# Performance work log

Hardware: AMD Instinct MI355X
Metric: run time of the kernel (lower is better)

The kernel has to match this reference:

```python
import jax, jax.numpy as jnp
import numpy as np

NUM_GROUPS = 32
EPS = 1e-6


def group_norm(x, w, b):
    # x: (B, C, L); normalize per group of C//32 channels over (channels-in-group, L)
    B, C, L = x.shape
    xg = x.reshape(B, NUM_GROUPS, C // NUM_GROUPS, L)
    mean = jnp.mean(xg, axis=(2, 3), keepdims=True)
    var = jnp.var(xg, axis=(2, 3), keepdims=True)
    xn = ((xg - mean) * jax.lax.rsqrt(var + EPS)).reshape(B, C, L)
    return xn * w[None, :, None] + b[None, :, None]


def conv1x1(x, w, b):
    # 1x1 Conv1d == channel-mixing linear. x: (B,C,L), w: (O,C), b: (O,)
    return jnp.einsum('oc,bcl->bol', w, x) + b[None, :, None]


def setup_inputs() -> dict:
    key = jax.random.key(0)
    ks = jax.random.split(key, 6)
    B, C, L = 8, 512, 2048
    s = 1.0 / np.sqrt(C)
    return {
        'x': jax.random.normal(ks[0], (B, C, L), dtype=jnp.float32),
        'gn_w': jnp.ones((C,), jnp.float32),
        'gn_b': jnp.zeros((C,), jnp.float32),
        'wq': jax.random.normal(ks[1], (C, C), dtype=jnp.float32) * s,
        'bq': jnp.zeros((C,), jnp.float32),
        'wk': jax.random.normal(ks[2], (C, C), dtype=jnp.float32) * s,
        'bk': jnp.zeros((C,), jnp.float32),
        'wv': jax.random.normal(ks[3], (C, C), dtype=jnp.float32) * s,
        'bv': jnp.zeros((C,), jnp.float32),
        'wo': jax.random.normal(ks[4], (C, C), dtype=jnp.float32) * s,
        'bo': jnp.zeros((C,), jnp.float32),
    }


def reference(x, gn_w, gn_b, wq, bq, wk, bk, wv, bv, wo, bo):
    B, C, L = x.shape
    h = group_norm(x, gn_w, gn_b)
    q = conv1x1(h, wq, bq)  # (B,C,L)
    k = conv1x1(h, wk, bk)
    v = conv1x1(h, wv, bv)
    scale = jnp.asarray(C, x.dtype) ** -0.5
    # scores over length: w[b,i,j] = sum_c q[b,c,i] k[b,c,j]
    w_ = jnp.einsum('bci,bcj->bij', q, k) * scale
    w_ = jax.nn.softmax(w_, axis=-1)
    # h[b,c,i] = sum_j w[b,i,j] v[b,c,j]
    h = jnp.einsum('bij,bcj->bci', w_, v)
    h = conv1x1(h, wo, bo)
    return x + h
```

## Files before the change

### kernel.cpp

```cpp
#include <hip/hip_runtime.h>
#include <math.h>

#define BATCH 8
#define CH 512
#define LEN 2048
#define NG 32
#define CPG 16

typedef unsigned short u16;
typedef __bf16 bf16x8 __attribute__((ext_vector_type(8)));
typedef float f32x16 __attribute__((ext_vector_type(16)));

__device__ __forceinline__ u16 f2bf(float f) {
    union { float f; unsigned u; } c; c.f = f;
    unsigned r = c.u + 0x7fffu + ((c.u >> 16) & 1u);
    return (u16)(r >> 16);
}
__device__ __forceinline__ float bf2f(u16 h) {
    union { unsigned u; float f; } c; c.u = ((unsigned)h) << 16;
    return c.f;
}
__device__ __forceinline__ void gload16(const u16* g, u16* l) {
    __builtin_amdgcn_global_load_lds(
        (const __attribute__((address_space(1))) unsigned int*)g,
        (__attribute__((address_space(3))) unsigned int*)l, 16, 0, 0);
}

__global__ __launch_bounds__(256) void zerof4(float4* __restrict__ p) {
    p[blockIdx.x * 256 + threadIdx.x] = make_float4(0.f, 0.f, 0.f, 0.f);
}

__global__ __launch_bounds__(256) void wconv4(const float* __restrict__ w0, const float* __restrict__ w1,
                                              const float* __restrict__ w2, const float* __restrict__ w3,
                                              u16* __restrict__ o0, u16* __restrict__ o1,
                                              u16* __restrict__ o2, u16* __restrict__ o3) {
    const float* s; u16* d;
    switch (blockIdx.y) {
        case 0: s = w0; d = o0; break;
        case 1: s = w1; d = o1; break;
        case 2: s = w2; d = o2; break;
        default: s = w3; d = o3; break;
    }
    const int i = blockIdx.x * 256 + threadIdx.x;
    float4 f = ((const float4*)s)[i];
    ushort4 o = make_ushort4(f2bf(f.x), f2bf(f.y), f2bf(f.z), f2bf(f.w));
    ((ushort4*)d)[i] = o;
}

__global__ __launch_bounds__(256) void gn_stats_p(const float* __restrict__ x,
                                                  float* __restrict__ stats) {
    const int blk = blockIdx.x;
    const int b = blk >> 7, g = (blk >> 2) & 31, sl = blk & 3;
    const float4* xp = (const float4*)(x + ((size_t)b * CH + (size_t)g * CPG) * LEN) + sl * 2048;
    float s = 0.f, s2 = 0.f;
    #pragma unroll
    for (int i = 0; i < 8; ++i) {
        float4 v = xp[threadIdx.x + i * 256];
        s += v.x + v.y + v.z + v.w;
        s2 = fmaf(v.x, v.x, fmaf(v.y, v.y, fmaf(v.z, v.z, fmaf(v.w, v.w, s2))));
    }
    #pragma unroll
    for (int off = 32; off > 0; off >>= 1) {
        s  += __shfl_down(s, off, 64);
        s2 += __shfl_down(s2, off, 64);
    }
    __shared__ float sm[2][4];
    const int lane = threadIdx.x & 63, wv = threadIdx.x >> 6;
    if (lane == 0) { sm[0][wv] = s; sm[1][wv] = s2; }
    __syncthreads();
    if (threadIdx.x == 0) {
        atomicAdd(&stats[b * NG + g],       sm[0][0] + sm[0][1] + sm[0][2] + sm[0][3]);
        atomicAdd(&stats[256 + b * NG + g], sm[1][0] + sm[1][1] + sm[1][2] + sm[1][3]);
    }
}

__global__ __launch_bounds__(256) void gn_fin(const float* __restrict__ stats,
                                              const float* __restrict__ gw,
                                              const float* __restrict__ gb,
                                              float* __restrict__ gnA,
                                              float* __restrict__ gnB) {
    const int idx = blockIdx.x * 256 + threadIdx.x;
    const int b = idx >> 9, c = idx & 511, g = c >> 4;
    const float S  = stats[b * NG + g];
    const float S2 = stats[256 + b * NG + g];
    const float mean = S * (1.f / (CPG * LEN));
    const float var  = S2 * (1.f / (CPG * LEN)) - mean * mean;
    const float a = rsqrtf(var + 1e-6f) * gw[c];
    gnA[idx] = a;
    gnB[idx] = gb[c] - mean * a;
}

__global__ __launch_bounds__(256) void gn_apply_t(const float* __restrict__ x,
                                                  const float* __restrict__ gnA,
                                                  const float* __restrict__ gnB,
                                                  u16* __restrict__ Ht) {
    __shared__ float tile[64][65];
    const int b = blockIdx.z, c0 = blockIdx.y * 64, l0 = blockIdx.x * 64;
    const int t = threadIdx.x, tl = t & 63, tr = t >> 6;
    #pragma unroll 4
    for (int i = 0; i < 16; ++i) {
        const int c = tr + i * 4;
        const float a = gnA[b * CH + c0 + c];
        const float sh = gnB[b * CH + c0 + c];
        tile[c][tl] = x[((size_t)b * CH + c0 + c) * LEN + l0 + tl] * a + sh;
    }
    __syncthreads();
    #pragma unroll 4
    for (int i = 0; i < 16; ++i) {
        const int l = tr + i * 4;
        Ht[((size_t)b * LEN + l0 + l) * CH + c0 + tl] = f2bf(tile[tl][l]);
    }
}

#define EPI_QK   0
#define EPI_TBN  1
#define EPI_EXP  2
#define EPI_TNRM 3
#define EPI_FIN  4

template <int MODE>
__global__ __launch_bounds__(256, 4) void gemm_bt(
    const u16* __restrict__ A, int lda, long long sA,
    const u16* __restrict__ B, int ldb, long long sB,
    void* __restrict__ Out, void* __restrict__ Out2,
    int ldo, long long sO,
    const float* __restrict__ bias, const float* __restrict__ bias2,
    const float* __restrict__ res, long long sR,
    float* __restrict__ rsum, long long sRS,
    int K, float alpha) {
    __shared__ u16 As[128 * 64];
    __shared__ u16 Bs[128 * 64];

    int bz, by, bx;
    if (MODE == EPI_EXP) {
        const int gx = gridDim.x, gy = gridDim.y;
        int flat = (blockIdx.z * gy + blockIdx.y) * gx + blockIdx.x;
        const int nbk = gx * gy * (int)gridDim.z;
        flat = (flat & 7) * (nbk >> 3) + (flat >> 3);
        bz = flat / (gx * gy);
        const int rr = flat - bz * gx * gy;
        by = rr / gx;
        bx = rr - by * gx;
    } else {
        bz = blockIdx.z; by = blockIdx.y; bx = blockIdx.x;
    }

    const int n0 = bx * 128, m0 = by * 128;
    A += (size_t)bz * sA;
    B += (size_t)bz * sB;
    const int t = threadIdx.x;
    const int lane = t & 63, wid = t >> 6;

    const int rowL = t >> 3, kq = (t & 7) ^ (rowL & 7);
    unsigned aoff = (unsigned)((m0 + rowL) * lda + kq * 8);
    unsigned boff = (unsigned)((n0 + rowL) * ldb + kq * 8);
    u16* const lds_dst_a = As + t * 8;
    u16* const lds_dst_b = Bs + t * 8;

    f32x16 acc[2][2];
    #pragma unroll
    for (int i = 0; i < 2; ++i)
        #pragma unroll
        for (int j = 0; j < 2; ++j)
            acc[i][j] = (f32x16)(0.f);

    const int col = lane & 31, half = lane >> 5;
    const int wm = (wid & 1) * 64, wn = (wid >> 1) * 64;
    const int mf = wm + col, nf = wn + col;
    const int mswz = mf & 7, nswz = nf & 7;

    for (int k0 = 0; k0 < K; k0 += 64) {
        #pragma unroll
        for (int g = 0; g < 4; ++g) {
            gload16(A + aoff + g * (32 * lda), lds_dst_a + g * 2048);
            gload16(B + boff + g * (32 * ldb), lds_dst_b + g * 2048);
        }
        aoff += 64; boff += 64;
        __syncthreads();
        #pragma unroll
        for (int ks = 0; ks < 4; ++ks) {
            const int kcA = ((ks * 2 + half) ^ mswz) * 8;
            const int kcB = ((ks * 2 + half) ^ nswz) * 8;
            bf16x8 a0 = *(const bf16x8*)(As + (mf)      * 64 + kcA);
            bf16x8 a1 = *(const bf16x8*)(As + (mf + 32) * 64 + kcA);
            bf16x8 b0 = *(const bf16x8*)(Bs + (nf)      * 64 + kcB);
            bf16x8 b1 = *(const bf16x8*)(Bs + (nf + 32) * 64 + kcB);
            acc[0][0] = __builtin_amdgcn_mfma_f32_32x32x16_bf16(a0, b0, acc[0][0], 0, 0, 0);
            acc[0][1] = __builtin_amdgcn_mfma_f32_32x32x16_bf16(a0, b1, acc[0][1], 0, 0, 0);
            acc[1][0] = __builtin_amdgcn_mfma_f32_32x32x16_bf16(a1, b0, acc[1][0], 0, 0, 0);
            acc[1][1] = __builtin_amdgcn_mfma_f32_32x32x16_bf16(a1, b1, acc[1][1], 0, 0, 0);
        }
        __syncthreads();
    }

    if (MODE == EPI_FIN) {
        float* O = (float*)Out + (size_t)bz * sO;
        const float* R = res + (size_t)bz * sR;
        #pragma unroll
        for (int im = 0; im < 2; ++im)
            #pragma unroll
            for (int g4 = 0; g4 < 4; ++g4) {
                const int mb = m0 + wm + im * 32 + g4 * 8 + half * 4;
                #pragma unroll
                for (int jn = 0; jn < 2; ++jn) {
                    const int n = n0 + wn + jn * 32 + col;
                    const float bb = bias[n];
                    const size_t base = (size_t)n * ldo + mb;
                    const float4 r4 = *(const float4*)&R[base];
                    float4 o4;
                    o4.x = acc[im][jn][g4 * 4 + 0] + bb + r4.x;
                    o4.y = acc[im][jn][g4 * 4 + 1] + bb + r4.y;
                    o4.z = acc[im][jn][g4 * 4 + 2] + bb + r4.z;
                    o4.w = acc[im][jn][g4 * 4 + 3] + bb + r4.w;
                    *(float4*)&O[base] = o4;
                }
            }
    } else if (MODE == EPI_EXP) {
        u16* O = (u16*)Out + (size_t)bz * sO;
        float* RS = rsum + (size_t)bz * sRS;
        float psum[2] = {0.f, 0.f};
        #pragma unroll
        for (int im = 0; im < 2; ++im)
            #pragma unroll
            for (int g4 = 0; g4 < 4; ++g4) {
                const int mb = m0 + wm + im * 32 + g4 * 8 + half * 4;
                #pragma unroll
                for (int jn = 0; jn < 2; ++jn) {
                    const int n = n0 + wn + jn * 32 + col;
                    u16 h0 = f2bf(__expf(acc[im][jn][g4 * 4 + 0] * alpha));
                    u16 h1 = f2bf(__expf(acc[im][jn][g4 * 4 + 1] * alpha));
                    u16 h2 = f2bf(__expf(acc[im][jn][g4 * 4 + 2] * alpha));
                    u16 h3 = f2bf(__expf(acc[im][jn][g4 * 4 + 3] * alpha));
                    psum[jn] += bf2f(h0) + bf2f(h1) + bf2f(h2) + bf2f(h3);
                    *(ushort4*)&O[(size_t)n * ldo + mb] = make_ushort4(h0, h1, h2, h3);
                }
            }
        #pragma unroll
        for (int jn = 0; jn < 2; ++jn) psum[jn] += __shfl_xor(psum[jn], 32, 64);
        if (half == 0) {
            #pragma unroll
            for (int jn = 0; jn < 2; ++jn)
                atomicAdd(&RS[n0 + wn + jn * 32 + col], psum[jn]);
        }
    } else {
        u16* O;
        const float* bi = bias;
        const float* RS = (MODE == EPI_TNRM) ? rsum + (size_t)bz * sRS : nullptr;
        int mbase = m0 + wm;
        if (MODE == EPI_QK) {
            const bool hi = (m0 & 512) != 0;
            O  = (u16*)(hi ? Out2 : Out) + (size_t)bz * sO;
            bi = hi ? bias2 : bias;
            mbase = (m0 & 511) + wm;
        } else {
            O = (u16*)Out + (size_t)bz * sO;
        }
        float inv[2];
        if (MODE == EPI_TNRM) {
            inv[0] = 1.f / RS[n0 + wn + col];
            inv[1] = 1.f / RS[n0 + wn + 32 + col];
        }
        #pragma unroll
        for (int im = 0; im < 2; ++im)
            #pragma unroll
            for (int g4 = 0; g4 < 4; ++g4) {
                const int mb = mbase + im * 32 + g4 * 8 + half * 4;
                float4 bm = make_float4(0.f, 0.f, 0.f, 0.f);
                if (MODE == EPI_QK) bm = *(const float4*)&bi[mb];
                #pragma unroll
                for (int jn = 0; jn < 2; ++jn) {
                    const int n = n0 + wn + jn * 32 + col;
                    float v0 = acc[im][jn][g4 * 4 + 0];
                    float v1 = acc[im][jn][g4 * 4 + 1];
                    float v2 = acc[im][jn][g4 * 4 + 2];
                    float v3 = acc[im][jn][g4 * 4 + 3];
                    if (MODE == EPI_QK)  { v0 += bm.x; v1 += bm.y; v2 += bm.z; v3 += bm.w; }
                    if (MODE == EPI_TBN) { const float bb = bi[n]; v0 += bb; v1 += bb; v2 += bb; v3 += bb; }
                    if (MODE == EPI_TNRM) { v0 *= inv[jn]; v1 *= inv[jn]; v2 *= inv[jn]; v3 *= inv[jn]; }
                    ushort4 pk = make_ushort4(f2bf(v0), f2bf(v1), f2bf(v2), f2bf(v3));
                    *(ushort4*)&O[(size_t)n * ldo + mb] = pk;
                }
            }
    }
}

extern "C" void kernel_launch(void* const* d_in, const int* in_sizes, int n_in,
                              void* d_out, int out_size, void* d_ws, size_t ws_size,
                              hipStream_t stream) {
    const float* x    = (const float*)d_in[0];
    const float* gn_w = (const float*)d_in[1];
    const float* gn_b = (const float*)d_in[2];
    const float* wq   = (const float*)d_in[3];
    const float* bq   = (const float*)d_in[4];
    const float* wk   = (const float*)d_in[5];
    const float* bk   = (const float*)d_in[6];
    const float* wv   = (const float*)d_in[7];
    const float* bv   = (const float*)d_in[8];
    const float* wo   = (const float*)d_in[9];
    const float* bo   = (const float*)d_in[10];
    float* out = (float*)d_out;

    char* p = (char*)d_ws;
    const size_t WSZ = (size_t)CH * CH * 2;
    const size_t HSZ = (size_t)BATCH * CH * LEN * 2;
    u16* Wqk = (u16*)p; p += 2 * WSZ;
    u16* Wvb = (u16*)p; p += WSZ;
    u16* Wob = (u16*)p; p += WSZ;
    u16* Ht  = (u16*)p; p += HSZ;
    u16* Qt  = (u16*)p; p += HSZ;
    u16* Kt  = (u16*)p; p += HSZ;
    u16* Vb  = (u16*)p; p += HSZ;
    u16* Sb  = (u16*)p; p += (size_t)BATCH * LEN * LEN * 2;
    float* gnA = (float*)p; p += (size_t)BATCH * CH * 4;
    float* gnB = (float*)p; p += (size_t)BATCH * CH * 4;
    float* rowsum = (float*)p; p += (size_t)BATCH * LEN * 4;
    float* stats  = (float*)p;

    const long long sH = (long long)LEN * CH;
    const long long sV = (long long)CH * LEN;
    const long long sS = (long long)LEN * LEN;
    const float scale = 0.04419417382415922f;

    zerof4<<<17, 256, 0, stream>>>((float4*)rowsum);
    wconv4<<<dim3(256, 4), 256, 0, stream>>>(wq, wk, wv, wo,
                                             Wqk, Wqk + (size_t)CH * CH, Wvb, Wob);
    gn_stats_p<<<BATCH * NG * 4, 256, 0, stream>>>(x, stats);
    gn_fin<<<BATCH * CH / 256, 256, 0, stream>>>(stats, gn_w, gn_b, gnA, gnB);
    gn_apply_t<<<dim3(LEN / 64, CH / 64, BATCH), 256, 0, stream>>>(x, gnA, gnB, Ht);

    gemm_bt<EPI_QK><<<dim3(16, 8, 8), 256, 0, stream>>>(
        Wqk, CH, 0, Ht, CH, sH, Qt, Kt, CH, sH, bq, bk, nullptr, 0, nullptr, 0, CH, 0.f);
    gemm_bt<EPI_TBN><<<dim3(4, 16, 8), 256, 0, stream>>>(
        Ht, CH, sH, Wvb, CH, 0, Vb, nullptr, LEN, sV, bv, nullptr, nullptr, 0, nullptr, 0, CH, 0.f);
    gemm_bt<EPI_EXP><<<dim3(16, 16, 8), 256, 0, stream>>>(
        Kt, CH, sH, Qt, CH, sH, Sb, nullptr, LEN, sS, nullptr, nullptr, nullptr, 0, rowsum, LEN, CH, scale);
    gemm_bt<EPI_TNRM><<<dim3(16, 4, 8), 256, 0, stream>>>(
        Vb, LEN, sV, Sb, LEN, sS, Ht, nullptr, CH, sH, nullptr, nullptr, nullptr, 0, rowsum, LEN, LEN, 0.f);
    gemm_bt<EPI_FIN><<<dim3(4, 16, 8), 256, 0, stream>>>(
        Ht, CH, sH, Wob, CH, 0, out, nullptr, LEN, sV, bo, nullptr, x, sV, nullptr, 0, CH, 0.f);
}
```

Baseline: 275.8 us.

## Fuse preprocessing kernels and fold group-norm finalize into the transpose-apply kernel

```diff
diff --git a/kernel.cpp b/kernel.cpp
--- a/kernel.cpp
+++ b/kernel.cpp
@@ -26,89 +26,94 @@
         (__attribute__((address_space(3))) unsigned int*)l, 16, 0, 0);
 }
 
-__global__ __launch_bounds__(256) void zerof4(float4* __restrict__ p) {
-    p[blockIdx.x * 256 + threadIdx.x] = make_float4(0.f, 0.f, 0.f, 0.f);
-}
-
-__global__ __launch_bounds__(256) void wconv4(const float* __restrict__ w0, const float* __restrict__ w1,
-                                              const float* __restrict__ w2, const float* __restrict__ w3,
-                                              u16* __restrict__ o0, u16* __restrict__ o1,
-                                              u16* __restrict__ o2, u16* __restrict__ o3) {
-    const float* s; u16* d;
-    switch (blockIdx.y) {
-        case 0: s = w0; d = o0; break;
-        case 1: s = w1; d = o1; break;
-        case 2: s = w2; d = o2; break;
-        default: s = w3; d = o3; break;
-    }
-    const int i = blockIdx.x * 256 + threadIdx.x;
-    float4 f = ((const float4*)s)[i];
-    ushort4 o = make_ushort4(f2bf(f.x), f2bf(f.y), f2bf(f.z), f2bf(f.w));
-    ((ushort4*)d)[i] = o;
-}
-
-__global__ __launch_bounds__(256) void gn_stats_p(const float* __restrict__ x,
-                                                  float* __restrict__ stats) {
+__global__ __launch_bounds__(256) void fused_pre(
+    const float* __restrict__ x,
+    const float* __restrict__ w0, const float* __restrict__ w1,
+    const float* __restrict__ w2, const float* __restrict__ w3,
+    u16* __restrict__ o0, u16* __restrict__ o1,
+    u16* __restrict__ o2, u16* __restrict__ o3,
+    float4* __restrict__ zbuf, float* __restrict__ stats) {
     const int blk = blockIdx.x;
-    const int b = blk >> 7, g = (blk >> 2) & 31, sl = blk & 3;
-    const float4* xp = (const float4*)(x + ((size_t)b * CH + (size_t)g * CPG) * LEN) + sl * 2048;
-    float s = 0.f, s2 = 0.f;
-    #pragma unroll
-    for (int i = 0; i < 8; ++i) {
-        float4 v = xp[threadIdx.x + i * 256];
-        s += v.x + v.y + v.z + v.w;
-        s2 = fmaf(v.x, v.x, fmaf(v.y, v.y, fmaf(v.z, v.z, fmaf(v.w, v.w, s2))));
-    }
-    #pragma unroll
-    for (int off = 32; off > 0; off >>= 1) {
-        s  += __shfl_down(s, off, 64);
-        s2 += __shfl_down(s2, off, 64);
-    }
-    __shared__ float sm[2][4];
-    const int lane = threadIdx.x & 63, wv = threadIdx.x >> 6;
-    if (lane == 0) { sm[0][wv] = s; sm[1][wv] = s2; }
-    __syncthreads();
-    if (threadIdx.x == 0) {
-        atomicAdd(&stats[b * NG + g],       sm[0][0] + sm[0][1] + sm[0][2] + sm[0][3]);
-        atomicAdd(&stats[256 + b * NG + g], sm[1][0] + sm[1][1] + sm[1][2] + sm[1][3]);
-    }
-}
-
-__global__ __launch_bounds__(256) void gn_fin(const float* __restrict__ stats,
-                                              const float* __restrict__ gw,
-                                              const float* __restrict__ gb,
-                                              float* __restrict__ gnA,
-                                              float* __restrict__ gnB) {
-    const int idx = blockIdx.x * 256 + threadIdx.x;
-    const int b = idx >> 9, c = idx & 511, g = c >> 4;
-    const float S  = stats[b * NG + g];
-    const float S2 = stats[256 + b * NG + g];
-    const float mean = S * (1.f / (CPG * LEN));
-    const float var  = S2 * (1.f / (CPG * LEN)) - mean * mean;
-    const float a = rsqrtf(var + 1e-6f) * gw[c];
-    gnA[idx] = a;
-    gnB[idx] = gb[c] - mean * a;
+    if (blk < 16) {
+        zbuf[blk * 256 + threadIdx.x] = make_float4(0.f, 0.f, 0.f, 0.f);
+    } else if (blk < 1040) {
+        const int wb = blk - 16;
+        const float* s; u16* d;
+        switch (wb >> 8) {
+            case 0: s = w0; d = o0; break;
+            case 1: s = w1; d = o1; break;
+            case 2: s = w2; d = o2; break;
+            default: s = w3; d = o3; break;
+        }
+        const int i = (wb & 255) * 256 + threadIdx.x;
+        float4 f = ((const float4*)s)[i];
+        ((ushort4*)d)[i] = make_ushort4(f2bf(f.x), f2bf(f.y), f2bf(f.z), f2bf(f.w));
+    } else {
+        const int sb = blk - 1040;
+        const int b = sb >> 7, g = (sb >> 2) & 31, sl = sb & 3;
+        const float4* xp = (const float4*)(x + ((size_t)b * CH + (size_t)g * CPG) * LEN) + sl * 2048;
+        float s = 0.f, s2 = 0.f;
+        #pragma unroll
+        for (int i = 0; i < 8; ++i) {
+            float4 v = xp[threadIdx.x + i * 256];
+            s += v.x + v.y + v.z + v.w;
+            s2 = fmaf(v.x, v.x, fmaf(v.y, v.y, fmaf(v.z, v.z, fmaf(v.w, v.w, s2))));
+        }
+        #pragma unroll
+        for (int off = 32; off > 0; off >>= 1) {
+            s  += __shfl_down(s, off, 64);
+            s2 += __shfl_down(s2, off, 64);
+        }
+        __shared__ float sm[2][4];
+        const int lane = threadIdx.x & 63, wv = threadIdx.x >> 6;
+        if (lane == 0) { sm[0][wv] = s; sm[1][wv] = s2; }
+        __syncthreads();
+        if (threadIdx.x == 0) {
+            const int base = (b * NG + g) * 4 + sl;
+            stats[base]        = sm[0][0] + sm[0][1] + sm[0][2] + sm[0][3];
+            stats[1024 + base] = sm[1][0] + sm[1][1] + sm[1][2] + sm[1][3];
+        }
+    }
 }
 
 __global__ __launch_bounds__(256) void gn_apply_t(const float* __restrict__ x,
-                                                  const float* __restrict__ gnA,
-                                                  const float* __restrict__ gnB,
+                                                  const float* __restrict__ stats,
+                                                  const float* __restrict__ gw,
+                                                  const float* __restrict__ gb,
                                                   u16* __restrict__ Ht) {
     __shared__ float tile[64][65];
     const int b = blockIdx.z, c0 = blockIdx.y * 64, l0 = blockIdx.x * 64;
-    const int t = threadIdx.x, tl = t & 63, tr = t >> 6;
-    #pragma unroll 4
-    for (int i = 0; i < 16; ++i) {
-        const int c = tr + i * 4;
-        const float a = gnA[b * CH + c0 + c];
-        const float sh = gnB[b * CH + c0 + c];
-        tile[c][tl] = x[((size_t)b * CH + c0 + c) * LEN + l0 + tl] * a + sh;
+    const int t = threadIdx.x;
+    const int rid = t >> 4, q = t & 15;
+    const float inv = 1.f / (CPG * LEN);
+    #pragma unroll
+    for (int pass = 0; pass < 4; ++pass) {
+        const int c = rid + pass * 16;
+        const int ca = c0 + c;
+        const int base = (b * NG + (ca >> 4)) * 4;
+        const float S  = stats[base + 0] + stats[base + 1] + stats[base + 2] + stats[base + 3];
+        const float S2 = stats[1024 + base + 0] + stats[1024 + base + 1]
+                       + stats[1024 + base + 2] + stats[1024 + base + 3];
+        const float mean = S * inv;
+        const float var  = S2 * inv - mean * mean;
+        const float a  = rsqrtf(var + 1e-6f) * gw[ca];
+        const float sh = gb[ca] - mean * a;
+        const float4 v = *(const float4*)&x[((size_t)b * CH + ca) * LEN + l0 + q * 4];
+        tile[c][q * 4 + 0] = v.x * a + sh;
+        tile[c][q * 4 + 1] = v.y * a + sh;
+        tile[c][q * 4 + 2] = v.z * a + sh;
+        tile[c][q * 4 + 3] = v.w * a + sh;
     }
     __syncthreads();
-    #pragma unroll 4
-    for (int i = 0; i < 16; ++i) {
-        const int l = tr + i * 4;
-        Ht[((size_t)b * LEN + l0 + l) * CH + c0 + tl] = f2bf(tile[tl][l]);
+    #pragma unroll
+    for (int pass = 0; pass < 4; ++pass) {
+        const int l = rid + pass * 16;
+        ushort4 o;
+        o.x = f2bf(tile[q * 4 + 0][l]);
+        o.y = f2bf(tile[q * 4 + 1][l]);
+        o.z = f2bf(tile[q * 4 + 2][l]);
+        o.w = f2bf(tile[q * 4 + 3][l]);
+        *(ushort4*)&Ht[((size_t)b * LEN + l0 + l) * CH + c0 + q * 4] = o;
     }
 }
 
@@ -311,8 +316,6 @@
     u16* Kt  = (u16*)p; p += HSZ;
     u16* Vb  = (u16*)p; p += HSZ;
     u16* Sb  = (u16*)p; p += (size_t)BATCH * LEN * LEN * 2;
-    float* gnA = (float*)p; p += (size_t)BATCH * CH * 4;
-    float* gnB = (float*)p; p += (size_t)BATCH * CH * 4;
     float* rowsum = (float*)p; p += (size_t)BATCH * LEN * 4;
     float* stats  = (float*)p;
 
@@ -321,12 +324,10 @@
     const long long sS = (long long)LEN * LEN;
     const float scale = 0.04419417382415922f;
 
-    zerof4<<<17, 256, 0, stream>>>((float4*)rowsum);
-    wconv4<<<dim3(256, 4), 256, 0, stream>>>(wq, wk, wv, wo,
-                                             Wqk, Wqk + (size_t)CH * CH, Wvb, Wob);
-    gn_stats_p<<<BATCH * NG * 4, 256, 0, stream>>>(x, stats);
-    gn_fin<<<BATCH * CH / 256, 256, 0, stream>>>(stats, gn_w, gn_b, gnA, gnB);
-    gn_apply_t<<<dim3(LEN / 64, CH / 64, BATCH), 256, 0, stream>>>(x, gnA, gnB, Ht);
+    fused_pre<<<2064, 256, 0, stream>>>(x, wq, wk, wv, wo,
+                                        Wqk, Wqk + (size_t)CH * CH, Wvb, Wob,
+                                        (float4*)rowsum, stats);
+    gn_apply_t<<<dim3(LEN / 64, CH / 64, BATCH), 256, 0, stream>>>(x, stats, gn_w, gn_b, Ht);
 
     gemm_bt<EPI_QK><<<dim3(16, 8, 8), 256, 0, stream>>>(
         Wqk, CH, 0, Ht, CH, sH, Qt, Kt, CH, sH, bq, bk, nullptr, 0, nullptr, 0, CH, 0.f);
```

Measured after the change: 271.4 us. No clear change (-1.6%).
